# Optimization experiments

Hardware: AMD Instinct MI355X
Metric: run time of the kernel (lower is better)

The kernel has to match this reference:

```python
import jax, jax.numpy as jnp
import numpy as np

B, K, T, V, H = 32, 5, 20, 9488, 1024


def setup_inputs() -> dict:
    key = jax.random.key(0)
    k0, k1, k2, k3, k4 = jax.random.split(key, 5)
    logprobs = jax.nn.log_softmax(jax.random.normal(k0, (B * K, V), jnp.float32), -1)
    beam_seq = jax.random.randint(k1, (B, K, T), 0, V)
    beam_seq_logprobs = jax.random.normal(k2, (B, K, T, V), jnp.float32)
    beam_logprobs_sum = jax.random.normal(k3, (B, K), jnp.float32)
    state = jax.random.normal(k4, (2, B * K, H), jnp.float32)
    return {"logprobs": logprobs, "beam_seq": beam_seq,
            "beam_seq_logprobs": beam_seq_logprobs,
            "beam_logprobs_sum": beam_logprobs_sum, "state": state,
            "beam_size": K, "t": T}


def reference(logprobs, beam_seq, beam_seq_logprobs, beam_logprobs_sum, state, beam_size, t):
    # One beam_step of CaptionModel.beam_search.
    batch = beam_logprobs_sum.shape[0]
    vocab = logprobs.shape[-1]
    lp = logprobs.reshape(batch, -1, vocab)                  # [B, K, V]
    cand = beam_logprobs_sum[:, :, None] + lp                # [B, K, V]
    flat = cand.reshape(batch, -1)                           # [B, K*V]
    # torch.sort(desc)[:, :beam_size] == top_k (sorted descending)
    ys, ix = jax.lax.top_k(flat, beam_size)                  # [B, K]
    beam_ix = ix // vocab                                    # source beam  [B, K]
    selected_ix = ix % vocab                                 # chosen word  [B, K]
    brange = jnp.arange(batch)[:, None]
    state_ix = (beam_ix + brange * lp.shape[1]).reshape(-1)  # [B*K]

    if t > 0:
        beam_seq = beam_seq[brange, beam_ix]                             # [B, K, t]
        beam_seq_logprobs = beam_seq_logprobs[brange, beam_ix]           # [B, K, t, V]
    beam_seq = jnp.concatenate([beam_seq, selected_ix[:, :, None].astype(beam_seq.dtype)], -1)

    beam_logprobs_sum = (jnp.take_along_axis(beam_logprobs_sum, beam_ix, 1)
                         + jnp.take_along_axis(lp.reshape(batch, -1), ix, 1))  # [B, K]

    beam_lp = lp[brange, beam_ix]                            # [B, K, V]
    beam_seq_logprobs = jnp.concatenate([beam_seq_logprobs, beam_lp[:, :, None, :]], 2)

    new_state = state[:, state_ix]                           # [layers, B*K, H]
    return beam_seq, beam_seq_logprobs, beam_logprobs_sum, new_state
```

## Files before the change

kernel.cpp:

```cpp
#include <hip/hip_runtime.h>

#define BB 32
#define KK 5
#define TT 20
#define VV 9488
#define HH 1024
#define NSPLIT 16
#define CHUNK (VV / NSPLIT)

#define OFF1 3360
#define OFF2 31883040
#define OFF3 31883200

typedef float f4 __attribute__((ext_vector_type(4)));

__device__ __forceinline__ bool better(float av, int ai, float bv, int bi) {
    return (av > bv) || (av == bv && ai < bi);
}

__device__ __forceinline__ void insert5(float tv[5], int ti[5], float val, int idx) {
#pragma unroll
    for (int j = 4; j >= 1; --j) {
        bool bj  = better(val, idx, tv[j],   ti[j]);
        bool bj1 = better(val, idx, tv[j-1], ti[j-1]);
        float nv = bj ? (bj1 ? tv[j-1] : val) : tv[j];
        int   ni = bj ? (bj1 ? ti[j-1] : idx) : ti[j];
        tv[j] = nv; ti[j] = ni;
    }
    bool b0 = better(val, idx, tv[0], ti[0]);
    ti[0] = b0 ? idx : ti[0];
    tv[0] = b0 ? val : tv[0];
}

__device__ __forceinline__ void merge_sorted5(float av[5], int ai[5],
                                              const float bv[5], const int bi[5]) {
    float ov[5]; int oi[5];
#pragma unroll
    for (int n = 0; n < 5; ++n) {
        float mv = 0.f; int mi = 0;
#pragma unroll
        for (int i = 0; i <= n; ++i) {
            const int j = n - i;
            float cv; int ci;
            if (better(av[i], ai[i], bv[j], bi[j])) { cv = av[i]; ci = ai[i]; }
            else                                    { cv = bv[j]; ci = bi[j]; }
            if (i == 0 || better(mv, mi, cv, ci)) { mv = cv; mi = ci; }
        }
        ov[n] = mv; oi[n] = mi;
    }
#pragma unroll
    for (int n = 0; n < 5; ++n) { av[n] = ov[n]; ai[n] = oi[n]; }
}

template<int MAXST>
__device__ __forceinline__ void wave_merge(float tv[5], int ti[5]) {
#pragma unroll
    for (int st = 1; st <= MAXST; st <<= 1) {
        float bv[5]; int bi[5];
#pragma unroll
        for (int j = 0; j < 5; ++j) {
            bv[j] = __shfl_xor(tv[j], st);
            bi[j] = __shfl_xor(ti[j], st);
        }
        merge_sorted5(tv, ti, bv, bi);
    }
}

__global__ __launch_bounds__(256) void topk_part_kernel(
    const float* __restrict__ logprobs,
    const float* __restrict__ sums,
    float* __restrict__ pv,
    int*   __restrict__ pi)
{
    const int b    = blockIdx.x / NSPLIT;
    const int part = blockIdx.x % NSPLIT;
    const int tid  = threadIdx.x;
    const int v0   = part * CHUNK;

    float tv[5]; int ti[5];
#pragma unroll
    for (int j = 0; j < 5; ++j) { tv[j] = -INFINITY; ti[j] = 0x7FFFFF00 + j; }

#pragma unroll
    for (int k = 0; k < KK; ++k) {
        const float s = sums[b * KK + k];
        const float* lp = logprobs + (size_t)(b * KK + k) * VV;
        for (int v = v0 + tid; v < v0 + CHUNK; v += 256)
            insert5(tv, ti, s + lp[v], k * VV + v);
    }

    wave_merge<32>(tv, ti);

    __shared__ float lv[4][5];
    __shared__ int   li[4][5];
    const int wid = tid >> 6, lane = tid & 63;
    if (lane == 0) {
#pragma unroll
        for (int j = 0; j < 5; ++j) { lv[wid][j] = tv[j]; li[wid][j] = ti[j]; }
    }
    __syncthreads();
    if (tid < 64) {
        if (tid < 4) {
#pragma unroll
            for (int j = 0; j < 5; ++j) { tv[j] = lv[tid][j]; ti[j] = li[tid][j]; }
        } else {
#pragma unroll
            for (int j = 0; j < 5; ++j) { tv[j] = -INFINITY; ti[j] = 0x7FFFFF00 + j; }
        }
        wave_merge<2>(tv, ti);
        if (tid == 0) {
#pragma unroll
            for (int j = 0; j < 5; ++j) {
                pv[(size_t)blockIdx.x * 5 + j] = tv[j];
                pi[(size_t)blockIdx.x * 5 + j] = ti[j];
            }
        }
    }
}

__global__ __launch_bounds__(256) void scatter_kernel(
    const float* __restrict__ logprobs,
    const int*   __restrict__ beam_seq_in,
    const float* __restrict__ bslp_in,
    const float* __restrict__ state_in,
    const float* __restrict__ pv,
    const int*   __restrict__ pi,
    float* __restrict__ out)
{
    const int bid  = blockIdx.x;
    const int tid  = threadIdx.x;
    const int lane = tid & 63;

    int b, k = 0, t = 0, role, r = 0;
    if (bid < 3360)      { role = 0; b = bid / 105; int rem = bid % 105; k = rem / 21; t = rem % 21; }
    else if (bid < 3680) { role = 1; r = bid - 3360; int i = r % 160; b = i / 5; k = i % 5; }
    else                 { role = 2; b = bid - 3680; }

    float tv[5]; int ti[5];
    if (lane < NSPLIT) {
        const size_t base = ((size_t)b * NSPLIT + lane) * 5;
#pragma unroll
        for (int j = 0; j < 5; ++j) { tv[j] = pv[base + j]; ti[j] = pi[base + j]; }
    } else {
#pragma unroll
        for (int j = 0; j < 5; ++j) { tv[j] = -INFINITY; ti[j] = 0x7FFFFF00 + j; }
    }
    wave_merge<32>(tv, ti);

    if (role == 0) {
        int sidx = 0;
#pragma unroll
        for (int j = 0; j < 5; ++j) if (k == j) sidx = ti[j];
        const int beam = sidx / VV;
        const float* src = (t < TT)
            ? bslp_in  + ((size_t)((b * KK + beam) * TT + t)) * VV
            : logprobs + (size_t)(b * KK + beam) * VV;
        const f4* s4 = (const f4*)src;
        f4* d4 = (f4*)(out + OFF1 + (size_t)bid * VV);
        for (int i = tid; i < VV / 4; i += 256) {
            f4 v = s4[i];
            __builtin_nontemporal_store(v, &d4[i]);
        }
    } else if (role == 1) {
        const int s = r / 160;
        int sidx = 0;
#pragma unroll
        for (int j = 0; j < 5; ++j) if (k == j) sidx = ti[j];
        const int beam = sidx / VV;
        const f4* s4 = (const f4*)(state_in + ((size_t)s * (BB * KK) + b * KK + beam) * HH);
        f4* d4 = (f4*)(out + OFF3 + (size_t)r * HH);
        for (int j = tid; j < HH / 4; j += 256) {
            f4 v = s4[j];
            __builtin_nontemporal_store(v, &d4[j]);
        }
    } else {
        if (tid < 105) {
            const int k2 = tid / 21, t2 = tid % 21;
            int sidx = 0;
#pragma unroll
            for (int j = 0; j < 5; ++j) if (k2 == j) sidx = ti[j];
            const int beam = sidx / VV;
            const int sel  = sidx - beam * VV;
            const int val  = (t2 < TT) ? beam_seq_in[(size_t)(b * KK + beam) * TT + t2] : sel;
            out[(size_t)b * 105 + tid] = (float)val;
        }
#pragma unroll
        for (int j = 0; j < 5; ++j)
            if (tid == 105 + j) out[OFF2 + b * KK + j] = tv[j];
    }
}

extern "C" void kernel_launch(void* const* d_in, const int* in_sizes, int n_in,
                              void* d_out, int out_size, void* d_ws, size_t ws_size,
                              hipStream_t stream) {
    const float* logprobs = (const float*)d_in[0];
    const int*   beam_seq = (const int*)  d_in[1];
    const float* bslp     = (const float*)d_in[2];
    const float* sums     = (const float*)d_in[3];
    const float* state    = (const float*)d_in[4];

    float* pv = (float*)d_ws;
    int*   pi = (int*)(pv + BB * NSPLIT * 5);
    float* out = (float*)d_out;

    topk_part_kernel<<<BB * NSPLIT, 256, 0, stream>>>(logprobs, sums, pv, pi);

    const int nblocks = 3360 + 320 + 32;
    scatter_kernel<<<nblocks, 256, 0, stream>>>(logprobs, beam_seq, bslp, state,
                                                pv, pi, out);
}
```

Before: 65.75 us.

## Move final top-k merge into its own kernel and drop nontemporal stores

Adds a small merge kernel that reduces the per-split top-k candidates once per batch and writes the beam index, word and score to workspace. The scatter kernel then reads those values instead of having every one of its ~3700 blocks redo the 16-way shuffle merge. It also replaces the nontemporal vector stores with plain stores and packs the small beam_seq and score outputs into a single block. The cost is one extra kernel launch and dependency, plus a serial single-block tail for the small outputs.

Measured after the change: 65.41 us. Within noise of the previous version (-0.5%).

```diff
diff --git a/kernel.cpp b/kernel.cpp
--- a/kernel.cpp
+++ b/kernel.cpp
@@ -118,75 +118,88 @@
     }
 }
 
+__global__ __launch_bounds__(64) void topk_merge_kernel(
+    const float* __restrict__ pv,
+    const int*   __restrict__ pi,
+    int*   __restrict__ ws_beam,
+    int*   __restrict__ ws_sel,
+    float* __restrict__ ws_sum)
+{
+    const int b   = blockIdx.x;
+    const int tid = threadIdx.x;
+
+    float tv[5]; int ti[5];
+    if (tid < NSPLIT) {
+        const size_t base = ((size_t)b * NSPLIT + tid) * 5;
+#pragma unroll
+        for (int j = 0; j < 5; ++j) { tv[j] = pv[base + j]; ti[j] = pi[base + j]; }
+    } else {
+#pragma unroll
+        for (int j = 0; j < 5; ++j) { tv[j] = -INFINITY; ti[j] = 0x7FFFFF00 + j; }
+    }
+
+    wave_merge<8>(tv, ti);
+
+    if (tid == 0) {
+#pragma unroll
+        for (int j = 0; j < 5; ++j) {
+            const int idx  = ti[j];
+            const int beam = idx / VV;
+            ws_beam[b * KK + j] = beam;
+            ws_sel [b * KK + j] = idx - beam * VV;
+            ws_sum [b * KK + j] = tv[j];
+        }
+    }
+}
+
 __global__ __launch_bounds__(256) void scatter_kernel(
     const float* __restrict__ logprobs,
     const int*   __restrict__ beam_seq_in,
     const float* __restrict__ bslp_in,
     const float* __restrict__ state_in,
-    const float* __restrict__ pv,
-    const int*   __restrict__ pi,
+    const int*   __restrict__ ws_beam,
+    const int*   __restrict__ ws_sel,
+    const float* __restrict__ ws_sum,
     float* __restrict__ out)
 {
-    const int bid  = blockIdx.x;
-    const int tid  = threadIdx.x;
-    const int lane = tid & 63;
-
-    int b, k = 0, t = 0, role, r = 0;
-    if (bid < 3360)      { role = 0; b = bid / 105; int rem = bid % 105; k = rem / 21; t = rem % 21; }
-    else if (bid < 3680) { role = 1; r = bid - 3360; int i = r % 160; b = i / 5; k = i % 5; }
-    else                 { role = 2; b = bid - 3680; }
-
-    float tv[5]; int ti[5];
-    if (lane < NSPLIT) {
-        const size_t base = ((size_t)b * NSPLIT + lane) * 5;
-#pragma unroll
-        for (int j = 0; j < 5; ++j) { tv[j] = pv[base + j]; ti[j] = pi[base + j]; }
-    } else {
-#pragma unroll
-        for (int j = 0; j < 5; ++j) { tv[j] = -INFINITY; ti[j] = 0x7FFFFF00 + j; }
-    }
-    wave_merge<32>(tv, ti);
-
-    if (role == 0) {
-        int sidx = 0;
-#pragma unroll
-        for (int j = 0; j < 5; ++j) if (k == j) sidx = ti[j];
-        const int beam = sidx / VV;
+    const int bid = blockIdx.x;
+    const int tid = threadIdx.x;
+    const int NROWS = BB * KK * (TT + 1);
+
+    if (bid < NROWS) {
+        const int b   = bid / (KK * (TT + 1));
+        const int rem = bid % (KK * (TT + 1));
+        const int k   = rem / (TT + 1);
+        const int t   = rem % (TT + 1);
+        const int beam = ws_beam[b * KK + k];
         const float* src = (t < TT)
             ? bslp_in  + ((size_t)((b * KK + beam) * TT + t)) * VV
             : logprobs + (size_t)(b * KK + beam) * VV;
         const f4* s4 = (const f4*)src;
         f4* d4 = (f4*)(out + OFF1 + (size_t)bid * VV);
-        for (int i = tid; i < VV / 4; i += 256) {
-            f4 v = s4[i];
-            __builtin_nontemporal_store(v, &d4[i]);
-        }
-    } else if (role == 1) {
-        const int s = r / 160;
-        int sidx = 0;
-#pragma unroll
-        for (int j = 0; j < 5; ++j) if (k == j) sidx = ti[j];
-        const int beam = sidx / VV;
+        for (int i = tid; i < VV / 4; i += 256) d4[i] = s4[i];
+    } else if (bid < NROWS + 2 * BB * KK) {
+        const int r = bid - NROWS;
+        const int s = r / (BB * KK);
+        const int i = r % (BB * KK);
+        const int b = i / KK;
+        const int beam = ws_beam[i];
         const f4* s4 = (const f4*)(state_in + ((size_t)s * (BB * KK) + b * KK + beam) * HH);
         f4* d4 = (f4*)(out + OFF3 + (size_t)r * HH);
-        for (int j = tid; j < HH / 4; j += 256) {
-            f4 v = s4[j];
-            __builtin_nontemporal_store(v, &d4[j]);
-        }
+        for (int j = tid; j < HH / 4; j += 256) d4[j] = s4[j];
     } else {
-        if (tid < 105) {
-            const int k2 = tid / 21, t2 = tid % 21;
-            int sidx = 0;
-#pragma unroll
-            for (int j = 0; j < 5; ++j) if (k2 == j) sidx = ti[j];
-            const int beam = sidx / VV;
-            const int sel  = sidx - beam * VV;
-            const int val  = (t2 < TT) ? beam_seq_in[(size_t)(b * KK + beam) * TT + t2] : sel;
-            out[(size_t)b * 105 + tid] = (float)val;
-        }
-#pragma unroll
-        for (int j = 0; j < 5; ++j)
-            if (tid == 105 + j) out[OFF2 + b * KK + j] = tv[j];
+        for (int j = tid; j < NROWS; j += 256) {
+            const int b   = j / (KK * (TT + 1));
+            const int rem = j % (KK * (TT + 1));
+            const int k   = rem / (TT + 1);
+            const int t   = rem % (TT + 1);
+            const int bk  = b * KK + k;
+            int val;
+            if (t < TT) val = beam_seq_in[(size_t)(b * KK + ws_beam[bk]) * TT + t];
+            else        val = ws_sel[bk];
+            out[j] = (float)val;
+        }
+        for (int j = tid; j < BB * KK; j += 256) out[OFF2 + j] = ws_sum[j];
     }
 }
 
@@ -199,13 +212,17 @@
     const float* sums     = (const float*)d_in[3];
     const float* state    = (const float*)d_in[4];
 
-    float* pv = (float*)d_ws;
-    int*   pi = (int*)(pv + BB * NSPLIT * 5);
-    float* out = (float*)d_out;
+    float* pv      = (float*)d_ws;
+    int*   pi      = (int*)(pv + BB * NSPLIT * 5);
+    int*   ws_beam = pi + BB * NSPLIT * 5;
+    int*   ws_sel  = ws_beam + BB * KK;
+    float* ws_sum  = (float*)(ws_sel + BB * KK);
+    float* out     = (float*)d_out;
 
     topk_part_kernel<<<BB * NSPLIT, 256, 0, stream>>>(logprobs, sums, pv, pi);
-
-    const int nblocks = 3360 + 320 + 32;
+    topk_merge_kernel<<<BB, 64, 0, stream>>>(pv, pi, ws_beam, ws_sel, ws_sum);
+
+    const int nblocks = 3360 + 320 + 1;
     scatter_kernel<<<nblocks, 256, 0, stream>>>(logprobs, beam_seq, bslp, state,
-                                                pv, pi, out);
-}
+                                                ws_beam, ws_sel, ws_sum, out);
+}
```

## Split scatter into merge kernel plus flat grid-stride gather copy via pointer table

Applied to the files above, without the earlier changes.

The two-kernel pipeline becomes three kernels. A small merge kernel computes the final top-5 per batch once and writes per-row source pointers into a workspace table. A flat grid-stride copy kernel then gathers every output row using that table, without the block-per-row layout and without the redundant top-k merging in every scatter block. The partial top-k kernel also changes: it uses early-exit insertion and a shared-memory tree reduction instead of wave shuffles. The cost is an extra launch, one more level of indirection in the copy, and plain stores in place of nontemporal ones.

After: 58.72 us. 1.12x faster.

```diff
diff --git a/kernel.cpp b/kernel.cpp
--- a/kernel.cpp
+++ b/kernel.cpp
@@ -12,58 +12,15 @@
 #define OFF2 31883040
 #define OFF3 31883200
 
+#define N1F4 7969920
+#define NSF4 81920
+#define TOTF4 (N1F4 + NSF4)
+
 typedef float f4 __attribute__((ext_vector_type(4)));
+typedef unsigned long long u64;
 
 __device__ __forceinline__ bool better(float av, int ai, float bv, int bi) {
     return (av > bv) || (av == bv && ai < bi);
-}
-
-__device__ __forceinline__ void insert5(float tv[5], int ti[5], float val, int idx) {
-#pragma unroll
-    for (int j = 4; j >= 1; --j) {
-        bool bj  = better(val, idx, tv[j],   ti[j]);
-        bool bj1 = better(val, idx, tv[j-1], ti[j-1]);
-        float nv = bj ? (bj1 ? tv[j-1] : val) : tv[j];
-        int   ni = bj ? (bj1 ? ti[j-1] : idx) : ti[j];
-        tv[j] = nv; ti[j] = ni;
-    }
-    bool b0 = better(val, idx, tv[0], ti[0]);
-    ti[0] = b0 ? idx : ti[0];
-    tv[0] = b0 ? val : tv[0];
-}
-
-__device__ __forceinline__ void merge_sorted5(float av[5], int ai[5],
-                                              const float bv[5], const int bi[5]) {
-    float ov[5]; int oi[5];
-#pragma unroll
-    for (int n = 0; n < 5; ++n) {
-        float mv = 0.f; int mi = 0;
-#pragma unroll
-        for (int i = 0; i <= n; ++i) {
-            const int j = n - i;
-            float cv; int ci;
-            if (better(av[i], ai[i], bv[j], bi[j])) { cv = av[i]; ci = ai[i]; }
-            else                                    { cv = bv[j]; ci = bi[j]; }
-            if (i == 0 || better(mv, mi, cv, ci)) { mv = cv; mi = ci; }
-        }
-        ov[n] = mv; oi[n] = mi;
-    }
-#pragma unroll
-    for (int n = 0; n < 5; ++n) { av[n] = ov[n]; ai[n] = oi[n]; }
-}
-
-template<int MAXST>
-__device__ __forceinline__ void wave_merge(float tv[5], int ti[5]) {
-#pragma unroll
-    for (int st = 1; st <= MAXST; st <<= 1) {
-        float bv[5]; int bi[5];
-#pragma unroll
-        for (int j = 0; j < 5; ++j) {
-            bv[j] = __shfl_xor(tv[j], st);
-            bi[j] = __shfl_xor(ti[j], st);
-        }
-        merge_sorted5(tv, ti, bv, bi);
-    }
 }
 
 __global__ __launch_bounds__(256) void topk_part_kernel(
@@ -81,112 +38,172 @@
 #pragma unroll
     for (int j = 0; j < 5; ++j) { tv[j] = -INFINITY; ti[j] = 0x7FFFFF00 + j; }
 
-#pragma unroll
     for (int k = 0; k < KK; ++k) {
         const float s = sums[b * KK + k];
         const float* lp = logprobs + (size_t)(b * KK + k) * VV;
-        for (int v = v0 + tid; v < v0 + CHUNK; v += 256)
-            insert5(tv, ti, s + lp[v], k * VV + v);
-    }
-
-    wave_merge<32>(tv, ti);
-
-    __shared__ float lv[4][5];
-    __shared__ int   li[4][5];
-    const int wid = tid >> 6, lane = tid & 63;
-    if (lane == 0) {
-#pragma unroll
-        for (int j = 0; j < 5; ++j) { lv[wid][j] = tv[j]; li[wid][j] = ti[j]; }
-    }
-    __syncthreads();
-    if (tid < 64) {
-        if (tid < 4) {
-#pragma unroll
-            for (int j = 0; j < 5; ++j) { tv[j] = lv[tid][j]; ti[j] = li[tid][j]; }
-        } else {
-#pragma unroll
-            for (int j = 0; j < 5; ++j) { tv[j] = -INFINITY; ti[j] = 0x7FFFFF00 + j; }
-        }
-        wave_merge<2>(tv, ti);
-        if (tid == 0) {
-#pragma unroll
-            for (int j = 0; j < 5; ++j) {
-                pv[(size_t)blockIdx.x * 5 + j] = tv[j];
-                pi[(size_t)blockIdx.x * 5 + j] = ti[j];
+        for (int v = v0 + tid; v < v0 + CHUNK; v += 256) {
+            const float val = s + lp[v];
+            const int idx = k * VV + v;
+            if (better(val, idx, tv[4], ti[4])) {
+                int pos = 4;
+#pragma unroll
+                for (int j = 3; j >= 0; --j)
+                    if (better(val, idx, tv[j], ti[j])) pos = j;
+#pragma unroll
+                for (int j = 4; j > 0; --j) {
+                    if (j > pos) { tv[j] = tv[j-1]; ti[j] = ti[j-1]; }
+                }
+                tv[pos] = val; ti[pos] = idx;
             }
         }
     }
-}
-
-__global__ __launch_bounds__(256) void scatter_kernel(
+
+    __shared__ float sv[256 * 5];
+    __shared__ int   si[256 * 5];
+
+    for (int stride = 128; stride >= 1; stride >>= 1) {
+        if (tid >= stride && tid < 2 * stride) {
+#pragma unroll
+            for (int j = 0; j < 5; ++j) { sv[tid*5+j] = tv[j]; si[tid*5+j] = ti[j]; }
+        }
+        __syncthreads();
+        if (tid < stride) {
+            float bv[5]; int bi[5];
+#pragma unroll
+            for (int j = 0; j < 5; ++j) { bv[j] = sv[(tid+stride)*5+j]; bi[j] = si[(tid+stride)*5+j]; }
+            float ov[5]; int oi[5];
+            int ia = 0, ib = 0;
+#pragma unroll
+            for (int n = 0; n < 5; ++n) {
+                if (better(tv[ia], ti[ia], bv[ib], bi[ib])) { ov[n] = tv[ia]; oi[n] = ti[ia]; ++ia; }
+                else                                        { ov[n] = bv[ib]; oi[n] = bi[ib]; ++ib; }
+            }
+#pragma unroll
+            for (int j = 0; j < 5; ++j) { tv[j] = ov[j]; ti[j] = oi[j]; }
+        }
+        __syncthreads();
+    }
+
+    if (tid == 0) {
+#pragma unroll
+        for (int j = 0; j < 5; ++j) {
+            pv[(size_t)blockIdx.x * 5 + j] = tv[j];
+            pi[(size_t)blockIdx.x * 5 + j] = ti[j];
+        }
+    }
+}
+
+__device__ __forceinline__ void merge_sorted5(float av[5], int ai[5],
+                                              const float bv[5], const int bi[5]) {
+    float ov[5]; int oi[5];
+#pragma unroll
+    for (int n = 0; n < 5; ++n) {
+        float mv = 0.f; int mi = 0;
+#pragma unroll
+        for (int i = 0; i <= n; ++i) {
+            const int j = n - i;
+            float cv; int ci;
+            if (better(av[i], ai[i], bv[j], bi[j])) { cv = av[i]; ci = ai[i]; }
+            else                                    { cv = bv[j]; ci = bi[j]; }
+            if (i == 0 || better(mv, mi, cv, ci)) { mv = cv; mi = ci; }
+        }
+        ov[n] = mv; oi[n] = mi;
+    }
+#pragma unroll
+    for (int n = 0; n < 5; ++n) { av[n] = ov[n]; ai[n] = oi[n]; }
+}
+
+__global__ __launch_bounds__(64) void merge_kernel(
+    const float* __restrict__ pv,
+    const int*   __restrict__ pi,
     const float* __restrict__ logprobs,
     const int*   __restrict__ beam_seq_in,
     const float* __restrict__ bslp_in,
     const float* __restrict__ state_in,
-    const float* __restrict__ pv,
-    const int*   __restrict__ pi,
+    u64* __restrict__ srcrow,
+    u64* __restrict__ srcst,
     float* __restrict__ out)
 {
-    const int bid  = blockIdx.x;
-    const int tid  = threadIdx.x;
-    const int lane = tid & 63;
-
-    int b, k = 0, t = 0, role, r = 0;
-    if (bid < 3360)      { role = 0; b = bid / 105; int rem = bid % 105; k = rem / 21; t = rem % 21; }
-    else if (bid < 3680) { role = 1; r = bid - 3360; int i = r % 160; b = i / 5; k = i % 5; }
-    else                 { role = 2; b = bid - 3680; }
+    const int b   = blockIdx.x;
+    const int tid = threadIdx.x;
 
     float tv[5]; int ti[5];
-    if (lane < NSPLIT) {
-        const size_t base = ((size_t)b * NSPLIT + lane) * 5;
+    if (tid < NSPLIT) {
+        const size_t base = ((size_t)b * NSPLIT + tid) * 5;
 #pragma unroll
         for (int j = 0; j < 5; ++j) { tv[j] = pv[base + j]; ti[j] = pi[base + j]; }
     } else {
 #pragma unroll
         for (int j = 0; j < 5; ++j) { tv[j] = -INFINITY; ti[j] = 0x7FFFFF00 + j; }
     }
-    wave_merge<32>(tv, ti);
-
-    if (role == 0) {
-        int sidx = 0;
-#pragma unroll
-        for (int j = 0; j < 5; ++j) if (k == j) sidx = ti[j];
-        const int beam = sidx / VV;
+
+#pragma unroll
+    for (int st = 1; st <= 8; st <<= 1) {
+        float bv[5]; int bi[5];
+#pragma unroll
+        for (int j = 0; j < 5; ++j) {
+            bv[j] = __shfl_xor(tv[j], st);
+            bi[j] = __shfl_xor(ti[j], st);
+        }
+        merge_sorted5(tv, ti, bv, bi);
+    }
+#pragma unroll
+    for (int j = 0; j < 5; ++j) {
+        tv[j] = __shfl(tv[j], 0);
+        ti[j] = __shfl(ti[j], 0);
+    }
+    int beam[5], sel[5];
+#pragma unroll
+    for (int j = 0; j < 5; ++j) { beam[j] = ti[j] / VV; sel[j] = ti[j] - beam[j] * VV; }
+
+    for (int rr = tid; rr < KK * (TT + 1); rr += 64) {
+        const int k = rr / (TT + 1), t = rr % (TT + 1);
+        int bm = 0, sl = 0;
+#pragma unroll
+        for (int j = 0; j < 5; ++j) if (k == j) { bm = beam[j]; sl = sel[j]; }
         const float* src = (t < TT)
-            ? bslp_in  + ((size_t)((b * KK + beam) * TT + t)) * VV
-            : logprobs + (size_t)(b * KK + beam) * VV;
-        const f4* s4 = (const f4*)src;
-        f4* d4 = (f4*)(out + OFF1 + (size_t)bid * VV);
-        for (int i = tid; i < VV / 4; i += 256) {
-            f4 v = s4[i];
-            __builtin_nontemporal_store(v, &d4[i]);
-        }
-    } else if (role == 1) {
-        const int s = r / 160;
-        int sidx = 0;
-#pragma unroll
-        for (int j = 0; j < 5; ++j) if (k == j) sidx = ti[j];
-        const int beam = sidx / VV;
-        const f4* s4 = (const f4*)(state_in + ((size_t)s * (BB * KK) + b * KK + beam) * HH);
-        f4* d4 = (f4*)(out + OFF3 + (size_t)r * HH);
-        for (int j = tid; j < HH / 4; j += 256) {
-            f4 v = s4[j];
-            __builtin_nontemporal_store(v, &d4[j]);
-        }
-    } else {
-        if (tid < 105) {
-            const int k2 = tid / 21, t2 = tid % 21;
-            int sidx = 0;
-#pragma unroll
-            for (int j = 0; j < 5; ++j) if (k2 == j) sidx = ti[j];
-            const int beam = sidx / VV;
-            const int sel  = sidx - beam * VV;
-            const int val  = (t2 < TT) ? beam_seq_in[(size_t)(b * KK + beam) * TT + t2] : sel;
-            out[(size_t)b * 105 + tid] = (float)val;
-        }
-#pragma unroll
-        for (int j = 0; j < 5; ++j)
-            if (tid == 105 + j) out[OFF2 + b * KK + j] = tv[j];
+            ? bslp_in  + ((size_t)((b * KK + bm) * TT + t)) * VV
+            : logprobs + (size_t)(b * KK + bm) * VV;
+        srcrow[b * KK * (TT + 1) + rr] = (u64)(uintptr_t)src;
+        const int val = (t < TT) ? beam_seq_in[(size_t)(b * KK + bm) * TT + t] : sl;
+        out[(size_t)b * KK * (TT + 1) + rr] = (float)val;
+    }
+
+    if (tid < 10) {
+        const int s = tid / 5, k = tid % 5;
+        int bm = 0;
+#pragma unroll
+        for (int j = 0; j < 5; ++j) if (k == j) bm = beam[j];
+        srcst[s * (BB * KK) + b * KK + k] =
+            (u64)(uintptr_t)(state_in + ((size_t)s * (BB * KK) + b * KK + bm) * HH);
+    }
+
+    if (tid == 0) {
+#pragma unroll
+        for (int j = 0; j < 5; ++j) out[OFF2 + b * KK + j] = tv[j];
+    }
+}
+
+__global__ __launch_bounds__(256) void copy_kernel(
+    const u64* __restrict__ srcrow,
+    const u64* __restrict__ srcst,
+    float* __restrict__ out)
+{
+    f4* __restrict__ dst1 = (f4*)(out + OFF1);
+    f4* __restrict__ dst3 = (f4*)(out + OFF3);
+    const int stride = gridDim.x * 256;
+    for (int idx = blockIdx.x * 256 + threadIdx.x; idx < TOTF4; idx += stride) {
+        if (idx < N1F4) {
+            const unsigned row = (unsigned)idx / 2372u;
+            const unsigned col = (unsigned)idx - row * 2372u;
+            const f4* __restrict__ s = (const f4*)(uintptr_t)srcrow[row];
+            dst1[idx] = s[col];
+        } else {
+            const int j = idx - N1F4;
+            const int r = j >> 8, col = j & 255;
+            const f4* __restrict__ s = (const f4*)(uintptr_t)srcst[r];
+            dst3[j] = s[col];
+        }
     }
 }
 
@@ -199,13 +216,14 @@
     const float* sums     = (const float*)d_in[3];
     const float* state    = (const float*)d_in[4];
 
-    float* pv = (float*)d_ws;
-    int*   pi = (int*)(pv + BB * NSPLIT * 5);
-    float* out = (float*)d_out;
+    u64*   srcrow = (u64*)d_ws;
+    u64*   srcst  = srcrow + BB * KK * (TT + 1);
+    float* pv     = (float*)(srcst + 2 * BB * KK);
+    int*   pi     = (int*)(pv + BB * NSPLIT * 5);
+    float* out    = (float*)d_out;
 
     topk_part_kernel<<<BB * NSPLIT, 256, 0, stream>>>(logprobs, sums, pv, pi);
-
-    const int nblocks = 3360 + 320 + 32;
-    scatter_kernel<<<nblocks, 256, 0, stream>>>(logprobs, beam_seq, bslp, state,
-                                                pv, pi, out);
-}
+    merge_kernel<<<BB, 64, 0, stream>>>(pv, pi, logprobs, beam_seq, bslp, state,
+                                        srcrow, srcst, out);
+    copy_kernel<<<2048, 256, 0, stream>>>(srcrow, srcst, out);
+}
```
